# Optimization experiments

Hardware: AMD Instinct MI355X
Metric: run time of the kernel (lower is better)

Reference implementation:

```python
import jax, jax.numpy as jnp
import numpy as np
import math

H = 8  # num_heads
SCALE = 1.0 / math.sqrt(512.0)  # original divides by sqrt(dim_V), not sqrt(head_dim)


def setup_inputs() -> dict:
    key = jax.random.key(0)
    ks = jax.random.split(key, 16)
    B, N, D = 32, 512, 512
    s = 1.0 / math.sqrt(D)
    return {
        "Q": jax.random.normal(ks[0], (B, N, D), jnp.float32),
        "K": jax.random.normal(ks[1], (B, N, D), jnp.float32),
        "Wq": jax.random.normal(ks[2], (D, D), jnp.float32) * s,
        "bq": jnp.zeros((D,), jnp.float32),
        "Wk": jax.random.normal(ks[3], (D, D), jnp.float32) * s,
        "bk": jnp.zeros((D,), jnp.float32),
        "Wv": jax.random.normal(ks[4], (D, D), jnp.float32) * s,
        "bv": jnp.zeros((D,), jnp.float32),
        "Wo": jax.random.normal(ks[5], (D, D), jnp.float32) * s,
        "bo": jnp.zeros((D,), jnp.float32),
        "W1": jax.random.normal(ks[6], (D, D), jnp.float32) * s,
        "b1": jnp.zeros((D,), jnp.float32),
        "W2": jax.random.normal(ks[7], (D, D), jnp.float32) * s,
        "b2": jnp.zeros((D,), jnp.float32),
    }


def reference(Q, K, Wq, bq, Wk, bk, Wv, bv, Wo, bo, W1, b1, W2, b2):
    B, Nq, D = Q.shape
    dh = D // H
    # projections (torch Linear: x @ W.T + b)
    q = (Q @ Wq.T + bq).reshape(B, Nq, H, dh)
    k = (K @ Wk.T + bk).reshape(B, K.shape[1], H, dh)
    v = (K @ Wv.T + bv).reshape(B, K.shape[1], H, dh)
    # scores: [B, H, Nq, Nk], scaled by 1/sqrt(dim_V)
    scores = jnp.einsum("bqhd,bkhd->bhqk", q, k) * SCALE
    # NOTE: original softmax is over dim=1 of [H*B, Nq, Nk] == the QUERY axis
    A = jax.nn.softmax(scores, axis=2)
    attn = jnp.einsum("bhqk,bkhd->bqhd", A, v).reshape(B, Nq, D)
    out = Q + (attn @ Wo.T + bo)  # dropout p=0.0
    ffn = jax.nn.relu(out @ W1.T + b1) @ W2.T + b2
    return out + ffn
```

## Files before the change

### kernel.cpp

```cpp
#include <hip/hip_runtime.h>
#include <stdint.h>

#define SCALE_ 0.044194173824159216f
#define QSC_ (0.044194173824159216f * 1.4426950408889634f)

typedef __attribute__((ext_vector_type(8))) short bf16x8;
typedef __attribute__((ext_vector_type(4))) float f32x4;

__device__ __forceinline__ ushort f2b(float f) {
  union { float f; uint32_t u; } v; v.f = f;
  return (ushort)((v.u + 0x7fffu + ((v.u >> 16) & 1u)) >> 16);
}
__device__ __forceinline__ uint32_t cvtpk(float lo, float hi) {
  uint32_t r; asm("v_cvt_pk_bf16_f32 %0, %1, %2" : "=v"(r) : "v"(lo), "v"(hi)); return r;
}
__device__ __forceinline__ float ex2(float x) {
  float r; asm("v_exp_f32 %0, %1" : "=v"(r) : "v"(x)); return r;
}
__device__ __forceinline__ void gld16(void* lds, const void* g) {
  __builtin_amdgcn_global_load_lds(
      (const __attribute__((address_space(1))) uint32_t*)g,
      (__attribute__((address_space(3))) uint32_t*)lds, 16, 0, 0);
}

__global__ __launch_bounds__(256)
void k_cvt(const float* __restrict__ Q, const float* __restrict__ K,
           const float* __restrict__ w0, const float* __restrict__ w1,
           const float* __restrict__ w2, const float* __restrict__ w3,
           const float* __restrict__ w4, const float* __restrict__ w5,
           ushort* __restrict__ Qb, ushort* __restrict__ Kb, ushort* __restrict__ Wb)
{
  const long long NQ = 8388608LL, NW = 262144LL;
  long long i = ((long long)blockIdx.x * 256 + threadIdx.x) * 4;
  const float* src; ushort* dst; long long off;
  if (i < NQ)        { src = Q; dst = Qb; off = i; }
  else if (i < 2*NQ) { src = K; dst = Kb; off = i - NQ; }
  else {
    long long j = i - 2*NQ; int seg = (int)(j / NW); off = j - (long long)seg * NW;
    switch (seg) { case 0: src = w0; break; case 1: src = w1; break; case 2: src = w2; break;
                   case 3: src = w3; break; case 4: src = w4; break; default: src = w5; }
    dst = Wb + (size_t)seg * NW;
  }
  float4 v = *(const float4*)(src + off);
  ushort4 o = make_ushort4(f2b(v.x), f2b(v.y), f2b(v.z), f2b(v.w));
  *(ushort4*)(dst + off) = o;
}

template<int EPI>
__device__ __forceinline__ void gemm_body(const ushort* __restrict__ A, const ushort* __restrict__ Bw,
                                          const float* __restrict__ bias, const float* __restrict__ extra,
                                          float* __restrict__ outf, ushort* __restrict__ outb,
                                          char* lds, int m0, int n0, float os)
{
  const int t = threadIdx.x;
  const int w = t >> 6, lane = t & 63;
  const int wm = w >> 1, wn = w & 1;
  const int rA = lane & 15, g = lane >> 4;

  const ushort* srcA[4]; int ldsA[4];
#pragma unroll
  for (int j = 0; j < 4; j++) {
    int L = (t + j*512) * 16;
    int U = L ^ (((L >> 7) & 7) << 4);
    srcA[j] = A + (size_t)(m0 + (U >> 7))*512 + ((U & 127) >> 1);
    ldsA[j] = L;
  }
  const ushort* srcB[2]; int ldsB[2];
#pragma unroll
  for (int j = 0; j < 2; j++) {
    int L = (t + j*512) * 16;
    int U = L ^ (((L >> 7) & 7) << 4);
    srcB[j] = Bw + (size_t)(n0 + (U >> 7))*512 + ((U & 127) >> 1);
    ldsB[j] = 32768 + L;
  }

#define STAGE_A(ti) do { char* bb_ = lds + ((ti) % 3) * 49152; \
    _Pragma("unroll") \
    for (int j = 0; j < 4; j++) gld16(bb_ + ldsA[j], srcA[j] + (ti)*64); } while (0)
#define STAGE_B(ti) do { char* bb_ = lds + ((ti) % 3) * 49152; \
    _Pragma("unroll") \
    for (int j = 0; j < 2; j++) gld16(bb_ + ldsB[j], srcB[j] + (ti)*64); } while (0)

  STAGE_A(0); STAGE_B(0);
  STAGE_A(1); STAGE_B(1);

  f32x4 acc[4][4] = {};
  for (int i = 0; i < 8; i++) {
    if (i < 7) asm volatile("s_waitcnt vmcnt(6)" ::: "memory");
    else       asm volatile("s_waitcnt vmcnt(0)" ::: "memory");
    __builtin_amdgcn_s_barrier();
    __builtin_amdgcn_sched_barrier(0);
    const char* bufc = lds + (i % 3) * 49152;

    bf16x8 afA[4], bfA[4];
#pragma unroll
    for (int m = 0; m < 4; m++) {
      int row = wm*64 + m*16 + rA;
      afA[m] = *(const bf16x8*)(bufc + ((row*128 + g*16) ^ ((row & 7) << 4)));
    }
#pragma unroll
    for (int n = 0; n < 4; n++) {
      int row = wn*64 + n*16 + rA;
      bfA[n] = *(const bf16x8*)(bufc + 32768 + ((row*128 + g*16) ^ ((row & 7) << 4)));
    }
    if (i < 6) STAGE_A(i + 2);
    __builtin_amdgcn_s_barrier();
    __builtin_amdgcn_sched_barrier(0);

    bf16x8 afB[4], bfB[4];
#pragma unroll
    for (int m = 0; m < 4; m++) {
      int row = wm*64 + m*16 + rA;
      afB[m] = *(const bf16x8*)(bufc + ((row*128 + 64 + g*16) ^ ((row & 7) << 4)));
    }
#pragma unroll
    for (int n = 0; n < 4; n++) {
      int row = wn*64 + n*16 + rA;
      bfB[n] = *(const bf16x8*)(bufc + 32768 + ((row*128 + 64 + g*16) ^ ((row & 7) << 4)));
    }
    if (i < 6) STAGE_B(i + 2);
    __builtin_amdgcn_s_setprio(1);
#pragma unroll
    for (int m = 0; m < 4; m++)
#pragma unroll
      for (int n = 0; n < 4; n++)
        acc[m][n] = __builtin_amdgcn_mfma_f32_16x16x32_bf16(afA[m], bfA[n], acc[m][n], 0, 0, 0);
    __builtin_amdgcn_s_setprio(0);
    __builtin_amdgcn_s_barrier();
    __builtin_amdgcn_sched_barrier(0);

    __builtin_amdgcn_s_setprio(1);
#pragma unroll
    for (int m = 0; m < 4; m++)
#pragma unroll
      for (int n = 0; n < 4; n++)
        acc[m][n] = __builtin_amdgcn_mfma_f32_16x16x32_bf16(afB[m], bfB[n], acc[m][n], 0, 0, 0);
    __builtin_amdgcn_s_setprio(0);
  }
#undef STAGE_A
#undef STAGE_B

#pragma unroll
  for (int m = 0; m < 4; m++)
#pragma unroll
    for (int n = 0; n < 4; n++) {
      int col = n0 + wn*64 + n*16 + rA;
      float bb = bias[col];
      if (EPI == 4) {
        int b = m0 >> 9, k0 = m0 & 511;
        int hh = col >> 6, dl = col & 63;
        int kg = k0 + wm*64 + m*16 + g*4;
        float v0 = acc[m][n][0] + bb, v1 = acc[m][n][1] + bb;
        float v2 = acc[m][n][2] + bb, v3 = acc[m][n][3] + bb;
        uint2 pk;
        pk.x = (uint32_t)f2b(v0) | ((uint32_t)f2b(v1) << 16);
        pk.y = (uint32_t)f2b(v2) | ((uint32_t)f2b(v3) << 16);
        *(uint2*)(outb + ((size_t)((b*8 + hh)*64 + dl)*512 + kg)) = pk;
      } else {
#pragma unroll
        for (int r = 0; r < 4; r++) {
          int row = m0 + wm*64 + m*16 + g*4 + r;
          size_t idx = (size_t)row*512 + col;
          float v = acc[m][n][r] + bb;
          if (EPI == 0)      outb[idx] = f2b(v * os);
          else if (EPI == 1) { float o = extra[idx] + v; outf[idx] = o; outb[idx] = f2b(o); }
          else if (EPI == 2) outb[idx] = f2b(v > 0.f ? v : 0.f);
          else               outf[idx] += v;
        }
      }
    }
}

template<int EPI>
__global__ __launch_bounds__(512, 2)
void k_gemm(const ushort* __restrict__ A, const ushort* __restrict__ Bw,
            const float* __restrict__ bias, const float* __restrict__ extra,
            float* __restrict__ outf, ushort* __restrict__ outb)
{
  __shared__ __align__(16) char lds[3*49152];
  gemm_body<EPI>(A, Bw, bias, extra, outf, outb, lds, blockIdx.x*256, blockIdx.y*128, 1.0f);
}

__global__ __launch_bounds__(512, 2)
void k_gemm_qkv(const ushort* __restrict__ Qb, const ushort* __restrict__ Kb,
                const ushort* __restrict__ Wb, const float* __restrict__ bq,
                const float* __restrict__ bk, const float* __restrict__ bvv,
                ushort* __restrict__ qkout, ushort* __restrict__ vpT)
{
  __shared__ __align__(16) char lds[3*49152];
  int z = blockIdx.z;
  if (z == 2) {
    gemm_body<4>(Kb, Wb + 2*(size_t)262144, bvv, nullptr, nullptr,
                 vpT, lds, blockIdx.x*256, blockIdx.y*128, 1.0f);
  } else {
    const ushort* A = (z == 0) ? Qb : Kb;
    const float* bias = (z == 0) ? bq : bk;
    float os = (z == 0) ? QSC_ : 1.0f;
    gemm_body<0>(A, Wb + (size_t)z*262144, bias, nullptr, nullptr,
                 qkout + (size_t)z*8388608, lds, blockIdx.x*256, blockIdx.y*128, os);
  }
}

__global__ __launch_bounds__(512, 2)
void k_att2(const ushort* __restrict__ qp, const ushort* __restrict__ kp,
            const ushort* __restrict__ vpT, float* __restrict__ zinv,
            ushort* __restrict__ attn)
{
  __shared__ __align__(16) char kt[65536];
  __shared__ __align__(16) char vt[65536];
  __shared__ __align__(16) char qpr[32768];
  int bh = blockIdx.x;
  int b = bh >> 3, h = bh & 7;
  int t = threadIdx.x, w = t >> 6, lane = t & 63;
  int rA = lane & 15, g = lane >> 4;
  const ushort* kbase = kp + (size_t)(b*512)*512 + h*64;
  const ushort* qbase = qp + (size_t)(b*512)*512 + h*64;
  const ushort* vbase = vpT + (size_t)bh*64*512;

#pragma unroll
  for (int i = 0; i < 8; i++) {
    int c = i*512 + t; int row = c >> 3, sl = c & 7;
    gld16(kt + c*16, kbase + (size_t)row*512 + ((sl ^ (row & 7))*8));
  }
#define STAGE_Q(buf, qb) do { \
    _Pragma("unroll") \
    for (int i = 0; i < 2; i++) { \
      int c = i*512 + t; int row = c >> 3, sl = c & 7; \
      gld16(qpr + (buf)*16384 + c*16, \
            qbase + (size_t)((qb)*128 + row)*512 + ((sl ^ (row & 7))*8)); } } while (0)
  STAGE_Q(0, 0);
  STAGE_Q(1, 1);
#pragma unroll
  for (int i = 0; i < 8; i++) {
    int c = i*512 + t; int d = c >> 6, sl = c & 63;
    gld16(vt + c*16, vbase + (size_t)d*512 + ((sl ^ (d & 7))*8));
  }

  asm volatile("s_waitcnt vmcnt(10)" ::: "memory");
  __builtin_amdgcn_s_barrier();
  __builtin_amdgcn_sched_barrier(0);
  bf16x8 kf[4][2];
#pragma unroll
  for (int n = 0; n < 4; n++)
#pragma unroll
    for (int ks = 0; ks < 2; ks++) {
      int k = w*64 + n*16 + rA;
      kf[n][ks] = *(const bf16x8*)(kt + k*128 + (((ks*4 + g) ^ (k & 7))*16));
    }
  float Zacc[4] = {0.f, 0.f, 0.f, 0.f};
  for (int qb = 0; qb < 4; qb++) {
    if (qb == 1)      { asm volatile("s_waitcnt vmcnt(10)" ::: "memory"); }
    else if (qb == 2) { asm volatile("s_waitcnt vmcnt(2)" ::: "memory"); }
    else if (qb == 3) { asm volatile("s_waitcnt vmcnt(0)" ::: "memory"); }
    if (qb) { __builtin_amdgcn_s_barrier(); __builtin_amdgcn_sched_barrier(0); }
    const char* qtb = qpr + (qb & 1)*16384;
    f32x4 acc[8][4] = {};
#pragma unroll
    for (int ks = 0; ks < 2; ks++) {
      bf16x8 af[8];
#pragma unroll
      for (int m = 0; m < 8; m++) {
        int q = m*16 + rA;
        af[m] = *(const bf16x8*)(qtb + q*128 + (((ks*4 + g) ^ (q & 7))*16));
      }
      __builtin_amdgcn_s_setprio(1);
#pragma unroll
      for (int m = 0; m < 8; m++)
#pragma unroll
        for (int n = 0; n < 4; n++)
          acc[m][n] = __builtin_amdgcn_mfma_f32_16x16x32_bf16(af[m], kf[n][ks], acc[m][n], 0, 0, 0);
      __builtin_amdgcn_s_setprio(0);
    }
    if (qb < 3) __builtin_amdgcn_s_barrier();
    if (qb < 2) STAGE_Q(qb & 1, qb + 2);
#pragma unroll
    for (int m = 0; m < 8; m++)
#pragma unroll
      for (int n = 0; n < 4; n++) {
        float s = 0.f;
#pragma unroll
        for (int r = 0; r < 4; r++) s += ex2(acc[m][n][r]);
        Zacc[n] += s;
      }
  }
#undef STAGE_Q
#pragma unroll
  for (int n = 0; n < 4; n++) {
    float v = Zacc[n];
    v += __shfl_xor(v, 16);
    v += __shfl_xor(v, 32);
    if (lane < 16) zinv[(size_t)bh*512 + w*64 + n*16 + lane] = 1.0f / v;
  }
  asm volatile("s_waitcnt vmcnt(0)" ::: "memory");
  __builtin_amdgcn_s_barrier();
  __builtin_amdgcn_sched_barrier(0);

  bf16x8 qf[4][2];
#pragma unroll
  for (int m = 0; m < 4; m++)
#pragma unroll
    for (int ks = 0; ks < 2; ks++)
      qf[m][ks] = *(const bf16x8*)(qbase + (size_t)(w*64 + m*16 + rA)*512 + ks*32 + g*8);
  char* Pw = qpr + w*4096;
  const float* zb = zinv + (size_t)bh*512;
  f32x4 oacc[4][4] = {};
  for (int kc = 0; kc < 16; kc++) {
    f32x4 sacc[2][4] = {};
#pragma unroll
    for (int ks = 0; ks < 2; ks++) {
      bf16x8 kfr[2];
#pragma unroll
      for (int kn = 0; kn < 2; kn++) {
        int k = kc*32 + kn*16 + rA;
        kfr[kn] = *(const bf16x8*)(kt + k*128 + (((ks*4 + g) ^ (k & 7))*16));
      }
      __builtin_amdgcn_s_setprio(1);
#pragma unroll
      for (int kn = 0; kn < 2; kn++)
#pragma unroll
        for (int m = 0; m < 4; m++)
          sacc[kn][m] = __builtin_amdgcn_mfma_f32_16x16x32_bf16(kfr[kn], qf[m][ks], sacc[kn][m], 0, 0, 0);
      __builtin_amdgcn_s_setprio(0);
    }
#pragma unroll
    for (int kn = 0; kn < 2; kn++) {
      f32x4 zv = *(const f32x4*)(zb + kc*32 + kn*16 + g*4);
#pragma unroll
      for (int m = 0; m < 4; m++) {
        float e0 = ex2(sacc[kn][m][0]) * zv[0];
        float e1 = ex2(sacc[kn][m][1]) * zv[1];
        float e2 = ex2(sacc[kn][m][2]) * zv[2];
        float e3 = ex2(sacc[kn][m][3]) * zv[3];
        uint2 pk; pk.x = cvtpk(e0, e1); pk.y = cvtpk(e2, e3);
        int q = m*16 + rA;
        *(uint2*)(Pw + q*64 + ((kn*32 + g*8) ^ ((q & 6) << 3))) = pk;
      }
    }
    bf16x8 pa[4], vb[4];
#pragma unroll
    for (int m = 0; m < 4; m++) {
      int q = m*16 + rA;
      pa[m] = *(const bf16x8*)(Pw + q*64 + ((g*16) ^ ((q & 6) << 3)));
    }
#pragma unroll
    for (int n = 0; n < 4; n++) {
      int d = n*16 + rA;
      vb[n] = *(const bf16x8*)(vt + d*1024 + ((kc*64 + g*16) ^ ((d & 7) << 4)));
    }
    __builtin_amdgcn_s_setprio(1);
#pragma unroll
    for (int m = 0; m < 4; m++)
#pragma unroll
      for (int n = 0; n < 4; n++)
        oacc[m][n] = __builtin_amdgcn_mfma_f32_16x16x32_bf16(pa[m], vb[n], oacc[m][n], 0, 0, 0);
    __builtin_amdgcn_s_setprio(0);
  }
#pragma unroll
  for (int m = 0; m < 4; m++)
#pragma unroll
    for (int n = 0; n < 4; n++)
#pragma unroll
      for (int r = 0; r < 4; r++) {
        int q = w*64 + m*16 + g*4 + r;
        int dcol = h*64 + n*16 + rA;
        attn[(size_t)(b*512 + q)*512 + dcol] = f2b(oacc[m][n][r]);
      }
}

extern "C" void kernel_launch(void* const* d_in, const int* in_sizes, int n_in,
                              void* d_out, int out_size, void* d_ws, size_t ws_size,
                              hipStream_t stream) {
  const float* Q  = (const float*)d_in[0];
  const float* K  = (const float*)d_in[1];
  const float* Wq = (const float*)d_in[2];
  const float* bq = (const float*)d_in[3];
  const float* Wk = (const float*)d_in[4];
  const float* bk = (const float*)d_in[5];
  const float* Wv = (const float*)d_in[6];
  const float* bv = (const float*)d_in[7];
  const float* Wo = (const float*)d_in[8];
  const float* bo = (const float*)d_in[9];
  const float* W1 = (const float*)d_in[10];
  const float* b1 = (const float*)d_in[11];
  const float* W2 = (const float*)d_in[12];
  const float* b2 = (const float*)d_in[13];
  float* out = (float*)d_out;

  const size_t SZ = (size_t)16384 * 512;
  ushort* Qb   = (ushort*)d_ws;
  ushort* Kb   = Qb + SZ;
  ushort* qp   = Kb + SZ;
  ushort* kp   = qp + SZ;
  ushort* vpT  = kp + SZ;
  ushort* Wb   = vpT + SZ;
  float*  zinv = (float*)(Wb + 6 * (size_t)262144);
  ushort* attn = Qb;
  ushort* outb = Kb;
  ushort* h1   = vpT;

  k_cvt<<<dim3(17920), dim3(256), 0, stream>>>(Q, K, Wq, Wk, Wv, Wo, W1, W2, Qb, Kb, Wb);
  k_gemm_qkv<<<dim3(64, 4, 3), dim3(512), 0, stream>>>(Qb, Kb, Wb, bq, bk, bv, qp, vpT);
  k_att2<<<dim3(256), dim3(512), 0, stream>>>(qp, kp, vpT, zinv, attn);
  k_gemm<1><<<dim3(64, 4), dim3(512), 0, stream>>>(attn, Wb + 3*(size_t)262144, bo, Q, out, outb);
  k_gemm<2><<<dim3(64, 4), dim3(512), 0, stream>>>(outb, Wb + 4*(size_t)262144, b1, nullptr, nullptr, h1);
  k_gemm<3><<<dim3(64, 4), dim3(512), 0, stream>>>(h1, Wb + 5*(size_t)262144, b2, nullptr, out, nullptr);
}
```

Measured before the change: 151.5 us.

## Use 32x32x16 MFMA with in-register P via permlane32 swap in attention

Rewrites the attention second pass to use 32x32x16 bf16 MFMA tiles instead of 16x16x32. The softmax probabilities now stay in registers and are rearranged into the A-operand layout with permlane32_swap, so the LDS write and read round-trip for P is gone. The normalizer reciprocals now sit in LDS rather than in a global zinv buffer. This cuts LDS traffic and global memory use, but adds register pressure from the 16-wide accumulators and depends on the lane mapping being exactly right.

Measured after the change: 148.3 us. 1.02x faster.

```diff
diff --git a/kernel.cpp b/kernel.cpp
--- a/kernel.cpp
+++ b/kernel.cpp
@@ -6,6 +6,8 @@
 
 typedef __attribute__((ext_vector_type(8))) short bf16x8;
 typedef __attribute__((ext_vector_type(4))) float f32x4;
+typedef __attribute__((ext_vector_type(16))) float f32x16;
+typedef __attribute__((ext_vector_type(2))) unsigned int uint2v;
 
 __device__ __forceinline__ ushort f2b(float f) {
   union { float f; uint32_t u; } v; v.f = f;
@@ -289,81 +291,78 @@
     float v = Zacc[n];
     v += __shfl_xor(v, 16);
     v += __shfl_xor(v, 32);
-    if (lane < 16) zinv[(size_t)bh*512 + w*64 + n*16 + lane] = 1.0f / v;
-  }
-  asm volatile("s_waitcnt vmcnt(0)" ::: "memory");
-  __builtin_amdgcn_s_barrier();
-  __builtin_amdgcn_sched_barrier(0);
-
-  bf16x8 qf[4][2];
-#pragma unroll
-  for (int m = 0; m < 4; m++)
-#pragma unroll
-    for (int ks = 0; ks < 2; ks++)
-      qf[m][ks] = *(const bf16x8*)(qbase + (size_t)(w*64 + m*16 + rA)*512 + ks*32 + g*8);
-  char* Pw = qpr + w*4096;
-  const float* zb = zinv + (size_t)bh*512;
-  f32x4 oacc[4][4] = {};
+    if (lane < 16) ((float*)qpr)[w*64 + n*16 + lane] = 1.0f / v;
+  }
+  __syncthreads();
+
+  const int l31 = lane & 31, hi5 = lane >> 5;
+  bf16x8 qf2[2][4];
+#pragma unroll
+  for (int qb = 0; qb < 2; qb++)
+#pragma unroll
+    for (int ksd = 0; ksd < 4; ksd++)
+      qf2[qb][ksd] = *(const bf16x8*)(qbase + (size_t)(w*64 + qb*32 + l31)*512 + ksd*16 + hi5*8);
+  const float* zl = (const float*)qpr;
+  f32x16 oacc[2][2] = {};
   for (int kc = 0; kc < 16; kc++) {
-    f32x4 sacc[2][4] = {};
-#pragma unroll
-    for (int ks = 0; ks < 2; ks++) {
-      bf16x8 kfr[2];
-#pragma unroll
-      for (int kn = 0; kn < 2; kn++) {
-        int k = kc*32 + kn*16 + rA;
-        kfr[kn] = *(const bf16x8*)(kt + k*128 + (((ks*4 + g) ^ (k & 7))*16));
-      }
+    bf16x8 kf2[4];
+#pragma unroll
+    for (int ksd = 0; ksd < 4; ksd++) {
+      int k = kc*32 + l31;
+      kf2[ksd] = *(const bf16x8*)(kt + k*128 + (((ksd*2 + hi5) ^ (k & 7))*16));
+    }
+    bf16x8 vf2[2][2];
+#pragma unroll
+    for (int db = 0; db < 2; db++)
+#pragma unroll
+      for (int ks = 0; ks < 2; ks++) {
+        int d = db*32 + l31;
+        vf2[db][ks] = *(const bf16x8*)(vt + d*1024 + (((kc*4 + ks*2 + hi5) ^ (d & 7))*16));
+      }
+    f32x4 zv[4];
+#pragma unroll
+    for (int j = 0; j < 4; j++)
+      zv[j] = *(const f32x4*)(zl + kc*32 + j*8 + hi5*4);
+#pragma unroll
+    for (int qb = 0; qb < 2; qb++) {
+      f32x16 s = {};
       __builtin_amdgcn_s_setprio(1);
 #pragma unroll
-      for (int kn = 0; kn < 2; kn++)
-#pragma unroll
-        for (int m = 0; m < 4; m++)
-          sacc[kn][m] = __builtin_amdgcn_mfma_f32_16x16x32_bf16(kfr[kn], qf[m][ks], sacc[kn][m], 0, 0, 0);
+      for (int ksd = 0; ksd < 4; ksd++)
+        s = __builtin_amdgcn_mfma_f32_32x32x16_bf16(kf2[ksd], qf2[qb][ksd], s, 0, 0, 0);
       __builtin_amdgcn_s_setprio(0);
-    }
-#pragma unroll
-    for (int kn = 0; kn < 2; kn++) {
-      f32x4 zv = *(const f32x4*)(zb + kc*32 + kn*16 + g*4);
-#pragma unroll
-      for (int m = 0; m < 4; m++) {
-        float e0 = ex2(sacc[kn][m][0]) * zv[0];
-        float e1 = ex2(sacc[kn][m][1]) * zv[1];
-        float e2 = ex2(sacc[kn][m][2]) * zv[2];
-        float e3 = ex2(sacc[kn][m][3]) * zv[3];
-        uint2 pk; pk.x = cvtpk(e0, e1); pk.y = cvtpk(e2, e3);
-        int q = m*16 + rA;
-        *(uint2*)(Pw + q*64 + ((kn*32 + g*8) ^ ((q & 6) << 3))) = pk;
-      }
-    }
-    bf16x8 pa[4], vb[4];
-#pragma unroll
-    for (int m = 0; m < 4; m++) {
-      int q = m*16 + rA;
-      pa[m] = *(const bf16x8*)(Pw + q*64 + ((g*16) ^ ((q & 6) << 3)));
-    }
-#pragma unroll
-    for (int n = 0; n < 4; n++) {
-      int d = n*16 + rA;
-      vb[n] = *(const bf16x8*)(vt + d*1024 + ((kc*64 + g*16) ^ ((d & 7) << 4)));
-    }
-    __builtin_amdgcn_s_setprio(1);
-#pragma unroll
-    for (int m = 0; m < 4; m++)
-#pragma unroll
-      for (int n = 0; n < 4; n++)
-        oacc[m][n] = __builtin_amdgcn_mfma_f32_16x16x32_bf16(pa[m], vb[n], oacc[m][n], 0, 0, 0);
-    __builtin_amdgcn_s_setprio(0);
-  }
-#pragma unroll
-  for (int m = 0; m < 4; m++)
-#pragma unroll
-    for (int n = 0; n < 4; n++)
-#pragma unroll
-      for (int r = 0; r < 4; r++) {
-        int q = w*64 + m*16 + g*4 + r;
-        int dcol = h*64 + n*16 + rA;
-        attn[(size_t)(b*512 + q)*512 + dcol] = f2b(oacc[m][n][r]);
+      float e[16];
+#pragma unroll
+      for (int r = 0; r < 16; r++) e[r] = ex2(s[r]) * zv[r >> 2][r & 3];
+      uint32_t x0 = cvtpk(e[0], e[1]),   y0 = cvtpk(e[4], e[5]);
+      uint32_t x1 = cvtpk(e[2], e[3]),   y1 = cvtpk(e[6], e[7]);
+      uint32_t x2 = cvtpk(e[8], e[9]),   y2 = cvtpk(e[12], e[13]);
+      uint32_t x3 = cvtpk(e[10], e[11]), y3 = cvtpk(e[14], e[15]);
+      uint2v r0 = __builtin_amdgcn_permlane32_swap(x0, y0, false, false);
+      uint2v r1 = __builtin_amdgcn_permlane32_swap(x1, y1, false, false);
+      uint2v r2 = __builtin_amdgcn_permlane32_swap(x2, y2, false, false);
+      uint2v r3 = __builtin_amdgcn_permlane32_swap(x3, y3, false, false);
+      union { uint32_t u[4]; bf16x8 v; } p0, p1;
+      p0.u[0] = r0[0]; p0.u[1] = r1[0]; p0.u[2] = r0[1]; p0.u[3] = r1[1];
+      p1.u[0] = r2[0]; p1.u[1] = r3[0]; p1.u[2] = r2[1]; p1.u[3] = r3[1];
+      __builtin_amdgcn_s_setprio(1);
+#pragma unroll
+      for (int db = 0; db < 2; db++) {
+        oacc[qb][db] = __builtin_amdgcn_mfma_f32_32x32x16_bf16(p0.v, vf2[db][0], oacc[qb][db], 0, 0, 0);
+        oacc[qb][db] = __builtin_amdgcn_mfma_f32_32x32x16_bf16(p1.v, vf2[db][1], oacc[qb][db], 0, 0, 0);
+      }
+      __builtin_amdgcn_s_setprio(0);
+    }
+  }
+#pragma unroll
+  for (int qb = 0; qb < 2; qb++)
+#pragma unroll
+    for (int db = 0; db < 2; db++)
+#pragma unroll
+      for (int r = 0; r < 16; r++) {
+        int q = w*64 + qb*32 + (r & 3) + 8*(r >> 2) + 4*hi5;
+        int d = db*32 + l31;
+        attn[(size_t)(b*512 + q)*512 + h*64 + d] = f2b(oacc[qb][db][r]);
       }
 }
 
```
